# Performance work log

Hardware: AMD Instinct MI355X
Metric: run time of the kernel (lower is better)

Reference implementation:

```python
import jax, jax.numpy as jnp
import numpy as np

B, G, T = 4096, 100, 24


def _greedy_dispatch(demand, caps, prices, slack_price):
    """Exact LP solution of: min prices@alloc + slack_price*slack
    s.t. 0<=alloc<=caps, sum(alloc)+slack = demand (per b,t).
    demand: [B,T] (nonneg), caps: [B,G,T], prices: [G], slack_price: scalar.
    Returns alloc [B,G,T], slack [B,T].
    """
    prices_all = jnp.concatenate([prices, slack_price[None]])        # [G+1]
    # slack capacity = demand itself (slack alone can absorb everything)
    caps_all = jnp.concatenate([caps, demand[:, None, :]], axis=1)    # [B,G+1,T]
    order = jnp.argsort(prices_all)                                   # merit order
    caps_s = caps_all[:, order, :]
    before = jnp.cumsum(caps_s, axis=1) - caps_s                      # capacity ahead in merit order
    alloc_s = jnp.clip(demand[:, None, :] - before, 0.0, caps_s)
    inv = jnp.argsort(order)
    alloc = alloc_s[:, inv, :]
    return alloc[:, :-1, :], alloc[:, -1, :]


def setup_inputs() -> dict:
    key = jax.random.key(0)
    k1, k2, k3, k4 = jax.random.split(key, 4)
    R_up = jax.random.uniform(k1, (B, G, T), dtype=jnp.float32)
    R_dn = jax.random.uniform(k2, (B, G, T), dtype=jnp.float32)
    omega_true = jax.random.normal(k3, (B, T), dtype=jnp.float32) * 5.0
    b_G = 10.0 + 40.0 * jax.random.uniform(k4, (G,), dtype=jnp.float32)  # marginal costs $/MWh
    return {
        "R_up": R_up,
        "R_dn": R_dn,
        "omega_true": omega_true,
        "b_G": b_G,
        "voll": jnp.float32(1000.0),
        "vosp": jnp.float32(500.0),
        "rt_up_ratio": jnp.float32(1.5),
        "rt_dn_ratio": jnp.float32(1.2),
    }


def reference(R_up, R_dn, omega_true, b_G, voll, vosp, rt_up_ratio, rt_dn_ratio):
    c_up = rt_up_ratio * b_G                                          # [G]
    c_dn = rt_dn_ratio * b_G                                          # [G]
    dem_up = jnp.maximum(omega_true, 0.0)                             # [B,T]
    dem_dn = jnp.maximum(-omega_true, 0.0)
    du, LS = _greedy_dispatch(dem_up, R_up, c_up, voll)
    dd, SP = _greedy_dispatch(dem_dn, R_dn, c_dn, vosp)
    rt_obj = (jnp.einsum('g,bgt->b', c_up, du)
              + jnp.einsum('g,bgt->b', c_dn, dd)
              + voll * LS.sum(axis=1) + vosp * SP.sum(axis=1))        # [B]
    return du, dd, LS, SP, rt_obj
```

## Files before the change

### kernel.cpp

```cpp
#include <hip/hip_runtime.h>

#define G_ 100
#define T_ 24
#define GP1 101
#define TILE (G_ * T_)
#define VPB (TILE / 4)
#define WPB 4
#define BLOCK (64 * WPB)

typedef float vfloat4 __attribute__((ext_vector_type(4)));

__global__ __launch_bounds__(BLOCK, 4) void dispatch_kernel(
    const float* __restrict__ R_up, const float* __restrict__ R_dn,
    const float* __restrict__ omega,
    const float* __restrict__ b_G, const float* __restrict__ voll,
    const float* __restrict__ vosp, const float* __restrict__ ru,
    const float* __restrict__ rd,
    float* __restrict__ out, int B)
{
    __shared__ float s_tile[WPB * TILE];
    __shared__ float s_obj[WPB];

    const int tid = threadIdx.x;

    float* s_praw = s_tile;
    int*   s_ord  = (int*)&s_tile[256];
    float* s_pr   = &s_tile[512];

    const int sp = tid >> 7;
    const int si = tid & 127;
    if (si < GP1) {
        float m;
        if (si < G_) m = (sp ? rd[0] : ru[0]) * b_G[si];
        else         m = sp ? vosp[0] : voll[0];
        s_praw[sp * GP1 + si] = m;
    }
    __syncthreads();
    if (si < GP1) {
        const float m = s_praw[sp * GP1 + si];
        int r = 0;
        for (int j = 0; j < GP1; ++j) {
            const float v = s_praw[sp * GP1 + j];
            r += (v < m) || (v == m && j < si);
        }
        s_ord[sp * 128 + r] = si;
        s_pr [sp * 128 + r] = m;
    }
    __syncthreads();

    const int w    = tid >> 6;
    const int lane = tid & 63;
    const int b = __builtin_amdgcn_readfirstlane(blockIdx.x * 2 + (w >> 1));
    const int p = __builtin_amdgcn_readfirstlane(w & 1);
    const size_t bgt = (size_t)B * TILE;

    const int hi_ok = (lane < GP1 - 64);
    const int   ord_lo = s_ord[p * 128 + lane];
    const int   ord_hi = hi_ok ? s_ord[p * 128 + 64 + lane] : 0;
    const float pr_lo  = s_pr [p * 128 + lane];
    const float pr_hi  = hi_ok ? s_pr [p * 128 + 64 + lane] : 0.f;
    __syncthreads();

    float* __restrict__ tw = &s_tile[w * TILE];
    {
        const vfloat4* __restrict__ s4 =
            (const vfloat4*)((p ? R_dn : R_up) + (size_t)b * TILE);
        vfloat4 v[9]; vfloat4 vt;
#pragma unroll
        for (int j = 0; j < 9; ++j) v[j] = s4[lane + j * 64];
        if (lane < VPB - 576) vt = s4[lane + 576];
#pragma unroll
        for (int j = 0; j < 9; ++j) *(vfloat4*)&tw[(lane + j * 64) * 4] = v[j];
        if (lane < VPB - 576) *(vfloat4*)&tw[(lane + 576) * 4] = vt;
    }
    asm volatile("s_waitcnt lgkmcnt(0)" ::: "memory");

    float objp = 0.f;
    if (lane < T_) {
        const int t = lane;
        const float om  = omega[(size_t)b * T_ + t];
        const float dem = p ? fmaxf(-om, 0.f) : fmaxf(om, 0.f);
        float before = 0.f;
#pragma unroll
        for (int r = 0; r < G_; ++r) {
            const int g = (r < 64) ? __builtin_amdgcn_readlane(ord_lo, r)
                                   : __builtin_amdgcn_readlane(ord_hi, r - 64);
            const float prr = (r < 64)
                ? __int_as_float(__builtin_amdgcn_readlane(__float_as_int(pr_lo), r))
                : __int_as_float(__builtin_amdgcn_readlane(__float_as_int(pr_hi), r - 64));
            const float cap = tw[g * T_ + t];
            const float a = fminf(fmaxf(dem - before, 0.f), cap);
            before += cap;
            objp = fmaf(prr, a, objp);
            tw[g * T_ + t] = a;
        }
        const float slack_pr =
            __int_as_float(__builtin_amdgcn_readlane(__float_as_int(pr_hi), GP1 - 1 - 64));
        const float slackv = fmaxf(dem - before, 0.f);
        objp = fmaf(slack_pr, slackv, objp);
        out[2 * bgt + (size_t)p * B * T_ + (size_t)b * T_ + t] = slackv;
    }

#pragma unroll
    for (int off = 32; off; off >>= 1) objp += __shfl_xor(objp, off, 64);
    if (lane == 0) s_obj[w] = objp;

    asm volatile("s_waitcnt lgkmcnt(0)" ::: "memory");
    {
        vfloat4* __restrict__ dst = (vfloat4*)out + ((size_t)p * B + b) * VPB;
#pragma unroll
        for (int j = 0; j < 9; ++j)
            dst[lane + j * 64] = *(const vfloat4*)&tw[(lane + j * 64) * 4];
        if (lane < VPB - 576)
            dst[lane + 576] = *(const vfloat4*)&tw[(lane + 576) * 4];
    }

    __syncthreads();
    if (tid == 0)
        out[2 * bgt + 2 * (size_t)B * T_ + b] = s_obj[0] + s_obj[1];
    if (tid == 128)
        out[2 * bgt + 2 * (size_t)B * T_ + b] = s_obj[2] + s_obj[3];
}

extern "C" void kernel_launch(void* const* d_in, const int* in_sizes, int n_in,
                              void* d_out, int out_size, void* d_ws, size_t ws_size,
                              hipStream_t stream)
{
    const float* R_up  = (const float*)d_in[0];
    const float* R_dn  = (const float*)d_in[1];
    const float* omega = (const float*)d_in[2];
    const float* b_G   = (const float*)d_in[3];
    const float* voll  = (const float*)d_in[4];
    const float* vosp  = (const float*)d_in[5];
    const float* ru    = (const float*)d_in[6];
    const float* rd    = (const float*)d_in[7];

    const int B = in_sizes[0] / TILE;
    float* out = (float*)d_out;

    dispatch_kernel<<<B / 2, BLOCK, 0, stream>>>(
        R_up, R_dn, omega, b_G, voll, vosp, ru, rd, out, B);
}
```

Baseline: 164.2 us.

## Issue global tile loads before price sort and batch LDS scan reads

Global loads of the capacity tile and omega now start before the in-block merit-order ranking, so memory latency overlaps the sort and its barriers. The per-column greedy scan is split into chunks of 16 that issue all LDS reads before the dependent arithmetic, which lets several LDS loads be in flight at once. The ranking loop is unrolled, and the explicit lgkmcnt waits become wave barriers. Holding the tile in registers across the sort raises register pressure, and the switch from waitcnt to wave_barrier relies on the compiler to order the LDS stores before the reads that follow.

```diff
diff --git a/kernel.cpp b/kernel.cpp
--- a/kernel.cpp
+++ b/kernel.cpp
@@ -10,6 +10,35 @@
 
 typedef float vfloat4 __attribute__((ext_vector_type(4)));
 
+template<int N>
+__device__ __forceinline__ void lds_scan_chunk(int k0,
+    float* __restrict__ tw, int t,
+    int ord_lo, int ord_hi, float pr_lo, float pr_hi,
+    float dem, float& before, float& objp)
+{
+    int gg[N]; float pr[N], cap[N];
+#pragma unroll
+    for (int j = 0; j < N; ++j) {
+        const int idx = k0 + j;
+        if (idx < 64) {
+            gg[j] = __builtin_amdgcn_readlane(ord_lo, idx);
+            pr[j] = __int_as_float(__builtin_amdgcn_readlane(__float_as_int(pr_lo), idx));
+        } else {
+            gg[j] = __builtin_amdgcn_readlane(ord_hi, idx - 64);
+            pr[j] = __int_as_float(__builtin_amdgcn_readlane(__float_as_int(pr_hi), idx - 64));
+        }
+    }
+#pragma unroll
+    for (int j = 0; j < N; ++j) cap[j] = tw[gg[j] * T_ + t];
+#pragma unroll
+    for (int j = 0; j < N; ++j) {
+        float a = fminf(fmaxf(dem - before, 0.f), cap[j]);
+        before += cap[j];
+        objp = fmaf(pr[j], a, objp);
+        tw[gg[j] * T_ + t] = a;
+    }
+}
+
 __global__ __launch_bounds__(BLOCK, 4) void dispatch_kernel(
     const float* __restrict__ R_up, const float* __restrict__ R_dn,
     const float* __restrict__ omega,
@@ -21,38 +50,48 @@
     __shared__ float s_tile[WPB * TILE];
     __shared__ float s_obj[WPB];
 
-    const int tid = threadIdx.x;
-
-    float* s_praw = s_tile;
-    int*   s_ord  = (int*)&s_tile[256];
-    float* s_pr   = &s_tile[512];
-
-    const int sp = tid >> 7;
-    const int si = tid & 127;
-    if (si < GP1) {
-        float m;
-        if (si < G_) m = (sp ? rd[0] : ru[0]) * b_G[si];
-        else         m = sp ? vosp[0] : voll[0];
-        s_praw[sp * GP1 + si] = m;
-    }
-    __syncthreads();
-    if (si < GP1) {
-        const float m = s_praw[sp * GP1 + si];
-        int r = 0;
-        for (int j = 0; j < GP1; ++j) {
-            const float v = s_praw[sp * GP1 + j];
-            r += (v < m) || (v == m && j < si);
-        }
-        s_ord[sp * 128 + r] = si;
-        s_pr [sp * 128 + r] = m;
-    }
-    __syncthreads();
-
+    const int tid  = threadIdx.x;
     const int w    = tid >> 6;
     const int lane = tid & 63;
     const int b = __builtin_amdgcn_readfirstlane(blockIdx.x * 2 + (w >> 1));
     const int p = __builtin_amdgcn_readfirstlane(w & 1);
     const size_t bgt = (size_t)B * TILE;
+
+    const vfloat4* __restrict__ s4 =
+        (const vfloat4*)((p ? R_dn : R_up) + (size_t)b * TILE);
+    vfloat4 v[9]; vfloat4 vt;
+#pragma unroll
+    for (int j = 0; j < 9; ++j) v[j] = s4[lane + j * 64];
+    if (lane < VPB - 576) vt = s4[lane + 576];
+    float om = 0.f;
+    if (lane < T_) om = omega[(size_t)b * T_ + lane];
+
+    float* s_praw = s_tile;
+    int*   s_ord  = (int*)&s_tile[256];
+    float* s_pr   = &s_tile[512];
+    {
+        const int sp = tid >> 7;
+        const int si = tid & 127;
+        if (si < GP1) {
+            float m;
+            if (si < G_) m = (sp ? rd[0] : ru[0]) * b_G[si];
+            else         m = sp ? vosp[0] : voll[0];
+            s_praw[sp * 128 + si] = m;
+        }
+        __syncthreads();
+        if (si < GP1) {
+            const float m = s_praw[sp * 128 + si];
+            int r = 0;
+#pragma unroll
+            for (int j = 0; j < GP1; ++j) {
+                const float vv = s_praw[sp * 128 + j];
+                r += (vv < m) || (vv == m && j < si);
+            }
+            s_ord[sp * 128 + r] = si;
+            s_pr [sp * 128 + r] = m;
+        }
+    }
+    __syncthreads();
 
     const int hi_ok = (lane < GP1 - 64);
     const int   ord_lo = s_ord[p * 128 + lane];
@@ -62,38 +101,24 @@
     __syncthreads();
 
     float* __restrict__ tw = &s_tile[w * TILE];
-    {
-        const vfloat4* __restrict__ s4 =
-            (const vfloat4*)((p ? R_dn : R_up) + (size_t)b * TILE);
-        vfloat4 v[9]; vfloat4 vt;
 #pragma unroll
-        for (int j = 0; j < 9; ++j) v[j] = s4[lane + j * 64];
-        if (lane < VPB - 576) vt = s4[lane + 576];
-#pragma unroll
-        for (int j = 0; j < 9; ++j) *(vfloat4*)&tw[(lane + j * 64) * 4] = v[j];
-        if (lane < VPB - 576) *(vfloat4*)&tw[(lane + 576) * 4] = vt;
-    }
-    asm volatile("s_waitcnt lgkmcnt(0)" ::: "memory");
+    for (int j = 0; j < 9; ++j) *(vfloat4*)&tw[(lane + j * 64) * 4] = v[j];
+    if (lane < VPB - 576) *(vfloat4*)&tw[(lane + 576) * 4] = vt;
+    __builtin_amdgcn_wave_barrier();
 
     float objp = 0.f;
     if (lane < T_) {
         const int t = lane;
-        const float om  = omega[(size_t)b * T_ + t];
         const float dem = p ? fmaxf(-om, 0.f) : fmaxf(om, 0.f);
         float before = 0.f;
-#pragma unroll
-        for (int r = 0; r < G_; ++r) {
-            const int g = (r < 64) ? __builtin_amdgcn_readlane(ord_lo, r)
-                                   : __builtin_amdgcn_readlane(ord_hi, r - 64);
-            const float prr = (r < 64)
-                ? __int_as_float(__builtin_amdgcn_readlane(__float_as_int(pr_lo), r))
-                : __int_as_float(__builtin_amdgcn_readlane(__float_as_int(pr_hi), r - 64));
-            const float cap = tw[g * T_ + t];
-            const float a = fminf(fmaxf(dem - before, 0.f), cap);
-            before += cap;
-            objp = fmaf(prr, a, objp);
-            tw[g * T_ + t] = a;
-        }
+        lds_scan_chunk<16>( 0, tw, t, ord_lo, ord_hi, pr_lo, pr_hi, dem, before, objp);
+        lds_scan_chunk<16>(16, tw, t, ord_lo, ord_hi, pr_lo, pr_hi, dem, before, objp);
+        lds_scan_chunk<16>(32, tw, t, ord_lo, ord_hi, pr_lo, pr_hi, dem, before, objp);
+        lds_scan_chunk<16>(48, tw, t, ord_lo, ord_hi, pr_lo, pr_hi, dem, before, objp);
+        lds_scan_chunk<16>(64, tw, t, ord_lo, ord_hi, pr_lo, pr_hi, dem, before, objp);
+        lds_scan_chunk<16>(80, tw, t, ord_lo, ord_hi, pr_lo, pr_hi, dem, before, objp);
+        lds_scan_chunk< 4>(96, tw, t, ord_lo, ord_hi, pr_lo, pr_hi, dem, before, objp);
+
         const float slack_pr =
             __int_as_float(__builtin_amdgcn_readlane(__float_as_int(pr_hi), GP1 - 1 - 64));
         const float slackv = fmaxf(dem - before, 0.f);
@@ -105,7 +130,7 @@
     for (int off = 32; off; off >>= 1) objp += __shfl_xor(objp, off, 64);
     if (lane == 0) s_obj[w] = objp;
 
-    asm volatile("s_waitcnt lgkmcnt(0)" ::: "memory");
+    __builtin_amdgcn_wave_barrier();
     {
         vfloat4* __restrict__ dst = (vfloat4*)out + ((size_t)p * B + b) * VPB;
 #pragma unroll
```

After: 159.6 us. -2.8%, faster.
